# Kernel tuning notes

Measured on AMD Instinct MI355X. Metric: run time of the kernel, lower is better.

The kernel has to match this reference:

```python
import jax, jax.numpy as jnp
import numpy as np

B, S, E, H = 2, 2048, 1024, 16
HD = E // H
CLAMP = 5.0


def setup_inputs() -> dict:
    key = jax.random.key(0)
    k1, k2, k3, k4 = jax.random.split(key, 4)
    # xavier-uniform-ish scale for weights
    lim_qkv = float(np.sqrt(6.0 / (E + 3 * E)))
    lim_o = float(np.sqrt(6.0 / (E + E)))
    return {
        "x": jax.random.normal(k1, (B, S, E), dtype=jnp.float32),
        "attn_bias": jax.random.normal(k2, (B, H, S, S), dtype=jnp.float32),
        "Wqkv": jax.random.uniform(k3, (3 * E, E), dtype=jnp.float32, minval=-lim_qkv, maxval=lim_qkv),
        "bqkv": jnp.zeros((3 * E,), dtype=jnp.float32),
        "Wo": jax.random.uniform(k4, (E, E), dtype=jnp.float32, minval=-lim_o, maxval=lim_o),
        "bo": jnp.zeros((E,), dtype=jnp.float32),
    }


def reference(x, attn_bias, Wqkv, bqkv, Wo, bo):
    b, s, e = x.shape
    # QKV projection: [B,S,3E] -> [B,S,H,3*HD] -> [B,H,S,3*HD]
    qkv = jnp.einsum("bse,fe->bsf", x, Wqkv) + bqkv
    qkv = qkv.reshape(b, s, H, 3 * HD).transpose(0, 2, 1, 3)
    q, k, v = jnp.split(qkv, 3, axis=-1)  # each [B,H,S,HD]
    # logits: bias added BEFORE 1/sqrt(d_k) scaling (as in source)
    logits = jnp.einsum("bhqd,bhkd->bhqk", q, k)
    logits = (logits + attn_bias) / jnp.sqrt(jnp.float32(HD))
    logits = jnp.clip(logits, -CLAMP, CLAMP)
    attn = jax.nn.softmax(logits, axis=-1)
    vals = jnp.einsum("bhqk,bhkd->bhqd", attn, v)
    vals = vals.transpose(0, 2, 1, 3).reshape(b, s, e)
    return jnp.einsum("bse,fe->bsf", vals, Wo) + bo
```

## Files before the change

### kernel.cpp

```cpp
#include <hip/hip_runtime.h>
#include <hip/hip_bf16.h>

#define NB 2
#define NS 2048
#define NE 1024
#define NH 16
#define HD 64

typedef __hip_bfloat16 bf16;
typedef __attribute__((ext_vector_type(8))) short bf16x8;
typedef __attribute__((ext_vector_type(4))) float f32x4;

typedef __attribute__((address_space(3))) void* lds_p;
typedef const __attribute__((address_space(1))) void* glb_p;

#define MFMA16(a, b, c) __builtin_amdgcn_mfma_f32_16x16x32_bf16((a), (b), (c), 0, 0, 0)

__device__ __forceinline__ void gl_lds16(const void* g, void* l) {
    __builtin_amdgcn_global_load_lds((glb_p)g, (lds_p)l, 16, 0, 0);
}

__device__ __forceinline__ bf16x8 ldv8(const bf16* p) { return *(const bf16x8*)p; }

__global__ __launch_bounds__(256) void cast3_k(const float* __restrict__ x,
                                               const float* __restrict__ wqkv,
                                               const float* __restrict__ wo,
                                               bf16* __restrict__ xb,
                                               bf16* __restrict__ wqkvb,
                                               bf16* __restrict__ wob) {
    const int n_x = NB * NS * NE / 4;
    const int n_q = 3 * NE * NE / 4;
    const int n_o = NE * NE / 4;
    int i = blockIdx.x * 256 + threadIdx.x;
    const float* in;
    bf16* out;
    int j;
    if (i < n_x) {
        in = x; out = xb; j = i;
    } else if (i < n_x + n_q) {
        in = wqkv; out = wqkvb; j = i - n_x;
    } else if (i < n_x + n_q + n_o) {
        in = wo; out = wob; j = i - n_x - n_q;
    } else {
        return;
    }
    float4 v = ((const float4*)in)[j];
    union { ushort4 u; bf16 b[4]; } pk;
    pk.b[0] = __float2bfloat16(v.x);
    pk.b[1] = __float2bfloat16(v.y);
    pk.b[2] = __float2bfloat16(v.z);
    pk.b[3] = __float2bfloat16(v.w);
    ((ushort4*)out)[j] = pk.u;
}

__global__ __launch_bounds__(256) void qkv_gemm(const bf16* __restrict__ A,
                                                const bf16* __restrict__ Bm,
                                                const float* __restrict__ bqkv,
                                                bf16* __restrict__ Qb, bf16* __restrict__ Kb,
                                                bf16* __restrict__ Vtb) {
    __shared__ bf16 As[128 * 32];
    __shared__ bf16 Bs[128 * 32];
    const int brow = blockIdx.x * 128;
    const int bcol = blockIdx.y * 128;
    const int t = threadIdx.x;
    const int w = t >> 6, lane = t & 63;
    const int wr = (w >> 1) * 64, wc = (w & 1) * 64;
    const int lr = lane & 15, lh = lane >> 4;
    const int K = 1024;

    f32x4 acc[4][4];
#pragma unroll
    for (int m = 0; m < 4; ++m)
#pragma unroll
        for (int n = 0; n < 4; ++n) acc[m][n] = (f32x4){0.f, 0.f, 0.f, 0.f};

    const bf16* ga0 = A + (size_t)(brow + (t >> 2)) * K + (t & 3) * 8;
    const bf16* ga1 = A + (size_t)(brow + 64 + (t >> 2)) * K + (t & 3) * 8;
    const bf16* gb0 = Bm + (size_t)(bcol + (t >> 2)) * K + (t & 3) * 8;
    const bf16* gb1 = Bm + (size_t)(bcol + 64 + (t >> 2)) * K + (t & 3) * 8;
    bf16* la0 = As + t * 8;
    bf16* la1 = As + 2048 + t * 8;
    bf16* lb0 = Bs + t * 8;
    bf16* lb1 = Bs + 2048 + t * 8;

    for (int kt = 0; kt < K; kt += 32) {
        gl_lds16(ga0 + kt, la0);
        gl_lds16(ga1 + kt, la1);
        gl_lds16(gb0 + kt, lb0);
        gl_lds16(gb1 + kt, lb1);
        __syncthreads();
        bf16x8 af[4], bfv[4];
#pragma unroll
        for (int m = 0; m < 4; ++m) af[m] = ldv8(&As[(wr + m * 16 + lr) * 32 + lh * 8]);
#pragma unroll
        for (int n = 0; n < 4; ++n) bfv[n] = ldv8(&Bs[(wc + n * 16 + lr) * 32 + lh * 8]);
#pragma unroll
        for (int m = 0; m < 4; ++m)
#pragma unroll
            for (int n = 0; n < 4; ++n) acc[m][n] = MFMA16(af[m], bfv[n], acc[m][n]);
        __syncthreads();
    }

#pragma unroll
    for (int n = 0; n < 4; ++n) {
        const int col = bcol + wc + n * 16 + lr;
        const int h = col / 192;
        const int r = col - h * 192;
        const int wh = r >> 6;
        const int d = r & 63;
        const float bq = bqkv[col];
#pragma unroll
        for (int m = 0; m < 4; ++m) {
            const int row0 = brow + wr + m * 16 + lh * 4;
            const int b = row0 >> 11;
            const int s0 = row0 & 2047;
            const size_t hb = (size_t)(b * NH + h) * (NS * HD);
            if (wh == 2) {
                alignas(8) bf16 tmp[4];
#pragma unroll
                for (int i = 0; i < 4; ++i) tmp[i] = __float2bfloat16(acc[m][n][i] + bq);
                *(ushort4*)(Vtb + hb + (size_t)d * NS + s0) = *(const ushort4*)tmp;
            } else {
                bf16* dst = (wh == 0 ? Qb : Kb) + hb + (size_t)s0 * HD + d;
#pragma unroll
                for (int i = 0; i < 4; ++i) dst[(size_t)i * HD] = __float2bfloat16(acc[m][n][i] + bq);
            }
        }
    }
}

__global__ __launch_bounds__(256, 3) void attn_k(const bf16* __restrict__ Qb,
                                                 const bf16* __restrict__ Kb,
                                                 const bf16* __restrict__ Vtb,
                                                 const float* __restrict__ bias,
                                                 bf16* __restrict__ valsb) {
    const int L = blockIdx.x;
    const int xcd = L & 7, kk = L >> 3;
    const int bh = (xcd << 2) | (kk >> 5);
    const int q0 = (kk & 31) * 64;
    const int t = threadIdx.x;
    const int w = t >> 6, lane = t & 63;
    const int lr = lane & 15, lh = lane >> 4;

    __shared__ bf16 Kls[2][64 * 64];
    __shared__ bf16 Vls[2][64 * 64];
    __shared__ bf16 Ps[4][16][72];

    const bf16* Qp = Qb + (size_t)bh * NS * HD;
    const bf16* Kp = Kb + (size_t)bh * NS * HD;
    const bf16* Vp = Vtb + (size_t)bh * HD * NS;

    const int qw = q0 + w * 16;
    bf16x8 qf0 = ldv8(&Qp[(qw + lr) * HD + lh * 8]);
    bf16x8 qf1 = ldv8(&Qp[(qw + lr) * HD + 32 + lh * 8]);

    const float* Bp = bias + (size_t)bh * NS * NS + (size_t)(qw + lr) * NS + lh * 4;

    const int srow0 = t >> 3;
    const int sce0 = ((t & 7) * 8) ^ ((srow0 & 7) << 3);
    const int srow1 = srow0 + 32;
    const int sce1 = ((t & 7) * 8) ^ ((srow1 & 7) << 3);

    f32x4 acc_o[4];
    float rowsum = 0.f;
#pragma unroll
    for (int n = 0; n < 4; ++n) acc_o[n] = (f32x4){0.f, 0.f, 0.f, 0.f};

    const float C1 = 0.18033688011112042f;
    const float C2 = 7.2134752044448170f;

    const int rswz = (lr & 7) << 3;
    const int ce0 = (lh * 8) ^ rswz;
    const int ce1 = (32 + lh * 8) ^ rswz;

    gl_lds16(Kp + (size_t)srow0 * HD + sce0, &Kls[0][t * 8]);
    gl_lds16(Kp + (size_t)srow1 * HD + sce1, &Kls[0][2048 + t * 8]);
    gl_lds16(Vp + (size_t)srow0 * NS + sce0, &Vls[0][t * 8]);
    gl_lds16(Vp + (size_t)srow1 * NS + sce1, &Vls[0][2048 + t * 8]);
    __builtin_amdgcn_sched_barrier(0);
    float4 bv0[4], bv1[4], bv2[4];
#pragma unroll
    for (int n = 0; n < 4; ++n) bv0[n] = *(const float4*)(Bp + n * 16);
    __builtin_amdgcn_sched_barrier(0);
#pragma unroll
    for (int n = 0; n < 4; ++n) bv1[n] = *(const float4*)(Bp + 64 + n * 16);
    __builtin_amdgcn_sched_barrier(0);
    asm volatile("s_waitcnt vmcnt(8)" ::: "memory");
    __builtin_amdgcn_sched_barrier(0);
    __builtin_amdgcn_s_barrier();
    __builtin_amdgcn_sched_barrier(0);

#define ATTN_COMPUTE(CUR)                                                             \
    {                                                                                 \
        const bf16* Kc = &Kls[CUR][0];                                                \
        f32x4 s[4];                                                                   \
        _Pragma("unroll") for (int n = 0; n < 4; ++n) {                               \
            bf16x8 k0 = ldv8(&Kc[(n * 16 + lr) * 64 + ce0]);                          \
            bf16x8 k1 = ldv8(&Kc[(n * 16 + lr) * 64 + ce1]);                          \
            s[n] = (f32x4){0.f, 0.f, 0.f, 0.f};                                       \
            s[n] = MFMA16(k0, qf0, s[n]);                                             \
            s[n] = MFMA16(k1, qf1, s[n]);                                             \
        }                                                                             \
        _Pragma("unroll") for (int n = 0; n < 4; ++n) {                               \
            union { ushort4 u; bf16 b[4]; } pk;                                       \
            _Pragma("unroll") for (int i = 0; i < 4; ++i) {                           \
                float bb = (i == 0   ? bv0[n].x                                       \
                            : i == 1 ? bv0[n].y                                       \
                            : i == 2 ? bv0[n].z                                       \
                                     : bv0[n].w);                                     \
                float xv = (s[n][i] + bb) * C1;                                       \
                xv = fminf(fmaxf(xv, -C2), C2);                                       \
                float p = exp2f(xv);                                                  \
                rowsum += p;                                                          \
                pk.b[i] = __float2bfloat16(p);                                        \
            }                                                                         \
            *(ushort4*)&Ps[w][lr][n * 16 + lh * 4] = pk.u;                            \
        }                                                                             \
        bf16x8 pa0 = ldv8(&Ps[w][lr][lh * 8]);                                        \
        bf16x8 pa1 = ldv8(&Ps[w][lr][32 + lh * 8]);                                   \
        const bf16* Vc = &Vls[CUR][0];                                                \
        _Pragma("unroll") for (int n = 0; n < 4; ++n) {                               \
            bf16x8 v0 = ldv8(&Vc[(n * 16 + lr) * 64 + ce0]);                          \
            bf16x8 v1 = ldv8(&Vc[(n * 16 + lr) * 64 + ce1]);                          \
            acc_o[n] = MFMA16(pa0, v0, acc_o[n]);                                     \
            acc_o[n] = MFMA16(pa1, v1, acc_o[n]);                                     \
        }                                                                             \
    }

    for (int tt = 0; tt < 30; ++tt) {
        const int cur = tt & 1;
        const int ktn = (tt + 1) * 64;
        {
            bf16* Kd = &Kls[cur ^ 1][0];
            bf16* Vd = &Vls[cur ^ 1][0];
            gl_lds16(Kp + (size_t)(ktn + srow0) * HD + sce0, Kd + t * 8);
            gl_lds16(Kp + (size_t)(ktn + srow1) * HD + sce1, Kd + 2048 + t * 8);
            gl_lds16(Vp + (size_t)srow0 * NS + ktn + sce0, Vd + t * 8);
            gl_lds16(Vp + (size_t)srow1 * NS + ktn + sce1, Vd + 2048 + t * 8);
        }
        __builtin_amdgcn_sched_barrier(0);
#pragma unroll
        for (int n = 0; n < 4; ++n) bv2[n] = *(const float4*)(Bp + ktn + 64 + n * 16);
        __builtin_amdgcn_sched_barrier(0);
        ATTN_COMPUTE(cur)
#pragma unroll
        for (int n = 0; n < 4; ++n) { bv0[n] = bv1[n]; bv1[n] = bv2[n]; }
        __builtin_amdgcn_sched_barrier(0);
        asm volatile("s_waitcnt vmcnt(4)" ::: "memory");
        __builtin_amdgcn_sched_barrier(0);
        __builtin_amdgcn_s_barrier();
        __builtin_amdgcn_sched_barrier(0);
    }

    {
        const int ktn = 31 * 64;
        bf16* Kd = &Kls[1][0];
        bf16* Vd = &Vls[1][0];
        gl_lds16(Kp + (size_t)(ktn + srow0) * HD + sce0, Kd + t * 8);
        gl_lds16(Kp + (size_t)(ktn + srow1) * HD + sce1, Kd + 2048 + t * 8);
        gl_lds16(Vp + (size_t)srow0 * NS + ktn + sce0, Vd + t * 8);
        gl_lds16(Vp + (size_t)srow1 * NS + ktn + sce1, Vd + 2048 + t * 8);
        __builtin_amdgcn_sched_barrier(0);
        ATTN_COMPUTE(0)
#pragma unroll
        for (int n = 0; n < 4; ++n) bv0[n] = bv1[n];
        __builtin_amdgcn_sched_barrier(0);
        asm volatile("s_waitcnt vmcnt(0)" ::: "memory");
        __builtin_amdgcn_sched_barrier(0);
        __builtin_amdgcn_s_barrier();
        __builtin_amdgcn_sched_barrier(0);
    }
    ATTN_COMPUTE(1)
#undef ATTN_COMPUTE

    rowsum += __shfl_xor(rowsum, 16, 64);
    rowsum += __shfl_xor(rowsum, 32, 64);
    float inv[4];
#pragma unroll
    for (int i = 0; i < 4; ++i) inv[i] = 1.0f / __shfl(rowsum, lh * 4 + i, 64);

    const int b = bh >> 4, h = bh & 15;
#pragma unroll
    for (int n = 0; n < 4; ++n) {
#pragma unroll
        for (int i = 0; i < 4; ++i) {
            const int qrow = qw + lh * 4 + i;
            valsb[(size_t)(b * NS + qrow) * NE + h * HD + n * 16 + lr] =
                __float2bfloat16(acc_o[n][i] * inv[i]);
        }
    }
}

__global__ __launch_bounds__(256) void out_gemm(const bf16* __restrict__ A,
                                                const bf16* __restrict__ Bm,
                                                const float* __restrict__ bo,
                                                float* __restrict__ out) {
    __shared__ bf16 As[128 * 32];
    __shared__ bf16 Bs[64 * 32];
    const int brow = blockIdx.x * 128;
    const int bcol = blockIdx.y * 64;
    const int t = threadIdx.x;
    const int w = t >> 6, lane = t & 63;
    const int wr = (w >> 1) * 64, wc = (w & 1) * 32;
    const int lr = lane & 15, lh = lane >> 4;
    const int K = 1024;

    f32x4 acc[4][2];
#pragma unroll
    for (int m = 0; m < 4; ++m)
#pragma unroll
        for (int n = 0; n < 2; ++n) acc[m][n] = (f32x4){0.f, 0.f, 0.f, 0.f};

    const bf16* ga0 = A + (size_t)(brow + (t >> 2)) * K + (t & 3) * 8;
    const bf16* ga1 = A + (size_t)(brow + 64 + (t >> 2)) * K + (t & 3) * 8;
    const bf16* gb0 = Bm + (size_t)(bcol + (t >> 2)) * K + (t & 3) * 8;
    bf16* la0 = As + t * 8;
    bf16* la1 = As + 2048 + t * 8;
    bf16* lb0 = Bs + t * 8;

    for (int kt = 0; kt < K; kt += 32) {
        gl_lds16(ga0 + kt, la0);
        gl_lds16(ga1 + kt, la1);
        gl_lds16(gb0 + kt, lb0);
        __syncthreads();
        bf16x8 af[4], bfv[2];
#pragma unroll
        for (int m = 0; m < 4; ++m) af[m] = ldv8(&As[(wr + m * 16 + lr) * 32 + lh * 8]);
#pragma unroll
        for (int n = 0; n < 2; ++n) bfv[n] = ldv8(&Bs[(wc + n * 16 + lr) * 32 + lh * 8]);
#pragma unroll
        for (int m = 0; m < 4; ++m)
#pragma unroll
            for (int n = 0; n < 2; ++n) acc[m][n] = MFMA16(af[m], bfv[n], acc[m][n]);
        __syncthreads();
    }

#pragma unroll
    for (int n = 0; n < 2; ++n) {
        const int col = bcol + wc + n * 16 + lr;
        const float bv = bo[col];
#pragma unroll
        for (int m = 0; m < 4; ++m) {
            const int row0 = brow + wr + m * 16 + lh * 4;
#pragma unroll
            for (int i = 0; i < 4; ++i) out[(size_t)(row0 + i) * NE + col] = acc[m][n][i] + bv;
        }
    }
}

extern "C" void kernel_launch(void* const* d_in, const int* in_sizes, int n_in,
                              void* d_out, int out_size, void* d_ws, size_t ws_size,
                              hipStream_t stream) {
    const float* x = (const float*)d_in[0];
    const float* attn_bias = (const float*)d_in[1];
    const float* Wqkv = (const float*)d_in[2];
    const float* bqkv = (const float*)d_in[3];
    const float* Wo = (const float*)d_in[4];
    const float* bo = (const float*)d_in[5];
    float* out = (float*)d_out;

    char* ws = (char*)d_ws;
    bf16* xb = (bf16*)(ws);
    bf16* Wqkvb = (bf16*)(ws + (8u << 20));
    bf16* Wob = (bf16*)(ws + (14u << 20));
    bf16* Qb = (bf16*)(ws + (16u << 20));
    bf16* Kb = (bf16*)(ws + (24u << 20));
    bf16* Vtb = (bf16*)(ws + (32u << 20));
    bf16* valsb = (bf16*)(ws + (40u << 20));

    cast3_k<<<8192, 256, 0, stream>>>(x, Wqkv, Wo, xb, Wqkvb, Wob);

    qkv_gemm<<<dim3(32, 24), 256, 0, stream>>>(xb, Wqkvb, bqkv, Qb, Kb, Vtb);

    attn_k<<<dim3(1024), 256, 0, stream>>>(Qb, Kb, Vtb, attn_bias, valsb);

    out_gemm<<<dim3(32, 16), 256, 0, stream>>>(valsb, Wob, bo, out);
}
```

Baseline: 245.4 us.

## Cut attention register pressure, swizzle P tile, raise occupancy to four blocks

Replaces the three rotating bias register buffers with two buffers named per unrolled step, so the loop is unrolled by two and each step refills the buffer it just consumed after its compute. Launch bounds rise from 3 to 4 blocks per SIMD, and the padded P staging array becomes an XOR-swizzled 64-wide layout to avoid bank conflicts without padding. This aims to lower VGPR and LDS usage so more waves can hide latency. The trade-off is that bias prefetch now has less lead time (issued after compute rather than before it), and a tighter register cap could cause spills.

```diff
diff --git a/kernel.cpp b/kernel.cpp
--- a/kernel.cpp
+++ b/kernel.cpp
@@ -129,7 +129,7 @@
     }
 }
 
-__global__ __launch_bounds__(256, 3) void attn_k(const bf16* __restrict__ Qb,
+__global__ __launch_bounds__(256, 4) void attn_k(const bf16* __restrict__ Qb,
                                                  const bf16* __restrict__ Kb,
                                                  const bf16* __restrict__ Vtb,
                                                  const float* __restrict__ bias,
@@ -144,7 +144,7 @@
 
     __shared__ bf16 Kls[2][64 * 64];
     __shared__ bf16 Vls[2][64 * 64];
-    __shared__ bf16 Ps[4][16][72];
+    __shared__ bf16 Ps[4][16 * 64];
 
     const bf16* Qp = Qb + (size_t)bh * NS * HD;
     const bf16* Kp = Kb + (size_t)bh * NS * HD;
@@ -172,25 +172,26 @@
     const int rswz = (lr & 7) << 3;
     const int ce0 = (lh * 8) ^ rswz;
     const int ce1 = (32 + lh * 8) ^ rswz;
+    const int pswz = (lr & 7) << 3;
 
     gl_lds16(Kp + (size_t)srow0 * HD + sce0, &Kls[0][t * 8]);
     gl_lds16(Kp + (size_t)srow1 * HD + sce1, &Kls[0][2048 + t * 8]);
     gl_lds16(Vp + (size_t)srow0 * NS + sce0, &Vls[0][t * 8]);
     gl_lds16(Vp + (size_t)srow1 * NS + sce1, &Vls[0][2048 + t * 8]);
     __builtin_amdgcn_sched_barrier(0);
-    float4 bv0[4], bv1[4], bv2[4];
-#pragma unroll
-    for (int n = 0; n < 4; ++n) bv0[n] = *(const float4*)(Bp + n * 16);
-    __builtin_amdgcn_sched_barrier(0);
-#pragma unroll
-    for (int n = 0; n < 4; ++n) bv1[n] = *(const float4*)(Bp + 64 + n * 16);
+    float4 bvA[4], bvB[4];
+#pragma unroll
+    for (int n = 0; n < 4; ++n) bvA[n] = *(const float4*)(Bp + n * 16);
+    __builtin_amdgcn_sched_barrier(0);
+#pragma unroll
+    for (int n = 0; n < 4; ++n) bvB[n] = *(const float4*)(Bp + 64 + n * 16);
     __builtin_amdgcn_sched_barrier(0);
     asm volatile("s_waitcnt vmcnt(8)" ::: "memory");
     __builtin_amdgcn_sched_barrier(0);
     __builtin_amdgcn_s_barrier();
     __builtin_amdgcn_sched_barrier(0);
 
-#define ATTN_COMPUTE(CUR)                                                             \
+#define ATTN_COMPUTE(CUR, BV)                                                         \
     {                                                                                 \
         const bf16* Kc = &Kls[CUR][0];                                                \
         f32x4 s[4];                                                                   \
@@ -204,20 +205,20 @@
         _Pragma("unroll") for (int n = 0; n < 4; ++n) {                               \
             union { ushort4 u; bf16 b[4]; } pk;                                       \
             _Pragma("unroll") for (int i = 0; i < 4; ++i) {                           \
-                float bb = (i == 0   ? bv0[n].x                                       \
-                            : i == 1 ? bv0[n].y                                       \
-                            : i == 2 ? bv0[n].z                                       \
-                                     : bv0[n].w);                                     \
+                float bb = (i == 0   ? BV[n].x                                        \
+                            : i == 1 ? BV[n].y                                        \
+                            : i == 2 ? BV[n].z                                        \
+                                     : BV[n].w);                                      \
                 float xv = (s[n][i] + bb) * C1;                                       \
                 xv = fminf(fmaxf(xv, -C2), C2);                                       \
                 float p = exp2f(xv);                                                  \
                 rowsum += p;                                                          \
                 pk.b[i] = __float2bfloat16(p);                                        \
             }                                                                         \
-            *(ushort4*)&Ps[w][lr][n * 16 + lh * 4] = pk.u;                            \
+            *(ushort4*)&Ps[w][lr * 64 + ((n * 16 + lh * 4) ^ pswz)] = pk.u;           \
         }                                                                             \
-        bf16x8 pa0 = ldv8(&Ps[w][lr][lh * 8]);                                        \
-        bf16x8 pa1 = ldv8(&Ps[w][lr][32 + lh * 8]);                                   \
+        bf16x8 pa0 = ldv8(&Ps[w][lr * 64 + ((lh * 8) ^ pswz)]);                       \
+        bf16x8 pa1 = ldv8(&Ps[w][lr * 64 + (((32 + lh * 8)) ^ pswz)]);                \
         const bf16* Vc = &Vls[CUR][0];                                                \
         _Pragma("unroll") for (int n = 0; n < 4; ++n) {                               \
             bf16x8 v0 = ldv8(&Vc[(n * 16 + lr) * 64 + ce0]);                          \
@@ -227,29 +228,30 @@
         }                                                                             \
     }
 
-    for (int tt = 0; tt < 30; ++tt) {
-        const int cur = tt & 1;
-        const int ktn = (tt + 1) * 64;
-        {
-            bf16* Kd = &Kls[cur ^ 1][0];
-            bf16* Vd = &Vls[cur ^ 1][0];
-            gl_lds16(Kp + (size_t)(ktn + srow0) * HD + sce0, Kd + t * 8);
-            gl_lds16(Kp + (size_t)(ktn + srow1) * HD + sce1, Kd + 2048 + t * 8);
-            gl_lds16(Vp + (size_t)srow0 * NS + ktn + sce0, Vd + t * 8);
-            gl_lds16(Vp + (size_t)srow1 * NS + ktn + sce1, Vd + 2048 + t * 8);
-        }
-        __builtin_amdgcn_sched_barrier(0);
-#pragma unroll
-        for (int n = 0; n < 4; ++n) bv2[n] = *(const float4*)(Bp + ktn + 64 + n * 16);
-        __builtin_amdgcn_sched_barrier(0);
-        ATTN_COMPUTE(cur)
-#pragma unroll
-        for (int n = 0; n < 4; ++n) { bv0[n] = bv1[n]; bv1[n] = bv2[n]; }
-        __builtin_amdgcn_sched_barrier(0);
-        asm volatile("s_waitcnt vmcnt(4)" ::: "memory");
-        __builtin_amdgcn_sched_barrier(0);
-        __builtin_amdgcn_s_barrier();
-        __builtin_amdgcn_sched_barrier(0);
+#define TILESTEP(CUR, BV, KTN)                                                        \
+    {                                                                                 \
+        bf16* Kd = &Kls[(CUR) ^ 1][0];                                                \
+        bf16* Vd = &Vls[(CUR) ^ 1][0];                                                \
+        gl_lds16(Kp + (size_t)((KTN) + srow0) * HD + sce0, Kd + t * 8);               \
+        gl_lds16(Kp + (size_t)((KTN) + srow1) * HD + sce1, Kd + 2048 + t * 8);        \
+        gl_lds16(Vp + (size_t)srow0 * NS + (KTN) + sce0, Vd + t * 8);                 \
+        gl_lds16(Vp + (size_t)srow1 * NS + (KTN) + sce1, Vd + 2048 + t * 8);          \
+        __builtin_amdgcn_sched_barrier(0);                                            \
+        ATTN_COMPUTE(CUR, BV)                                                         \
+        __builtin_amdgcn_sched_barrier(0);                                            \
+        _Pragma("unroll") for (int n = 0; n < 4; ++n)                                 \
+            BV[n] = *(const float4*)(Bp + (KTN) + 64 + n * 16);                       \
+        __builtin_amdgcn_sched_barrier(0);                                            \
+        asm volatile("s_waitcnt vmcnt(4)" ::: "memory");                              \
+        __builtin_amdgcn_sched_barrier(0);                                            \
+        __builtin_amdgcn_s_barrier();                                                 \
+        __builtin_amdgcn_sched_barrier(0);                                            \
+    }
+
+    for (int it = 0; it < 15; ++it) {
+        const int tt = it * 2;
+        TILESTEP(0, bvA, (tt + 1) * 64)
+        TILESTEP(1, bvB, (tt + 2) * 64)
     }
 
     {
@@ -261,16 +263,15 @@
         gl_lds16(Vp + (size_t)srow0 * NS + ktn + sce0, Vd + t * 8);
         gl_lds16(Vp + (size_t)srow1 * NS + ktn + sce1, Vd + 2048 + t * 8);
         __builtin_amdgcn_sched_barrier(0);
-        ATTN_COMPUTE(0)
-#pragma unroll
-        for (int n = 0; n < 4; ++n) bv0[n] = bv1[n];
+        ATTN_COMPUTE(0, bvA)
         __builtin_amdgcn_sched_barrier(0);
         asm volatile("s_waitcnt vmcnt(0)" ::: "memory");
         __builtin_amdgcn_sched_barrier(0);
         __builtin_amdgcn_s_barrier();
         __builtin_amdgcn_sched_barrier(0);
     }
-    ATTN_COMPUTE(1)
+    ATTN_COMPUTE(1, bvB)
+#undef TILESTEP
 #undef ATTN_COMPUTE
 
     rowsum += __shfl_xor(rowsum, 16, 64);
```

New measurement: 212.0 us. 13.6% less time.
